# Optimization experiments

Measured on AMD Instinct MI355X. Metric: run time of the kernel, lower is better.

Reference implementation:

```python
import jax, jax.numpy as jnp
import numpy as np

NUM_HEADS = 16


def setup_inputs() -> dict:
    key = jax.random.key(0)
    ks = jax.random.split(key, 5)
    B, S, D = 2, 2048, 1024
    x = jax.random.normal(ks[0], (B, S, D), dtype=jnp.float32)
    # torch Linear weights are [out_features, in_features]; y = x @ W.T + b
    Wq = jax.random.normal(ks[1], (D, D), dtype=jnp.float32) * (D ** -0.5)
    Wk = jax.random.normal(ks[2], (D, D), dtype=jnp.float32) * (D ** -0.5)
    Wv = jax.random.normal(ks[3], (D, D), dtype=jnp.float32) * (D ** -0.5)
    Wo = jax.random.normal(ks[4], (D, D), dtype=jnp.float32) * (D ** -0.5)
    bo = jnp.zeros((D,), dtype=jnp.float32)
    return {"x": x, "Wq": Wq, "Wk": Wk, "Wv": Wv, "Wo": Wo, "bo": bo}


def reference(x, Wq, Wk, Wv, Wo, bo):
    B, S, D = x.shape
    H = NUM_HEADS
    dh = D // H
    # projections (torch Linear: x @ W.T)
    q = (x @ Wq.T).reshape(B, S, H, dh).transpose(0, 2, 1, 3)  # [B,H,S,dh]
    k = (x @ Wk.T).reshape(B, S, H, dh).transpose(0, 2, 1, 3)
    v = (x @ Wv.T).reshape(B, S, H, dh).transpose(0, 2, 1, 3)
    # NOTE: original code takes shape[-1] of the TRANSPOSED key (n,H,dh,S),
    # so the softmax scale is seq_length**-0.5 (a bug we reproduce faithfully).
    scale = jnp.asarray(S, x.dtype) ** -0.5
    scores = jnp.einsum("bhqd,bhkd->bhqk", q, k)  # [B,H,S,S]
    causal = jnp.triu(jnp.ones((S, S), dtype=bool), k=1)
    scores = jnp.where(causal, -jnp.inf, scores * scale)
    weights = jax.nn.softmax(scores, axis=-1)
    # dropout p=0.0 -> identity
    ctx = jnp.einsum("bhqk,bhkd->bhqd", weights, v)  # [B,H,S,dh]
    ctx = ctx.transpose(0, 2, 1, 3).reshape(B, S, D)
    return ctx @ Wo.T + bo
```

## Files before the change

kernel.cpp:

```cpp
#include <hip/hip_runtime.h>
#include <hip/hip_bf16.h>

#define B_SZ    2
#define S_LEN   2048
#define D_MODEL 1024
#define H_NUM   16
#define DH      64
#define M_TOT   (B_SZ * S_LEN)

#define QSCALE (0.022097086912079608f * 1.4426950408889634f)

typedef __attribute__((ext_vector_type(8)))  short          bf16x8;
typedef __attribute__((ext_vector_type(4)))  float          f32x4;
typedef __attribute__((ext_vector_type(16))) float          f32x16;
typedef __attribute__((ext_vector_type(8)))  unsigned short u16x8;
typedef __attribute__((ext_vector_type(4)))  unsigned short u16x4;

__device__ inline unsigned short f2bf(float f) {
  unsigned int u = __float_as_uint(f);
  u += 0x7fffu + ((u >> 16) & 1u);
  return (unsigned short)(u >> 16);
}

__device__ inline float fexp2(float x) {
#if __has_builtin(__builtin_amdgcn_exp2f)
  return __builtin_amdgcn_exp2f(x);
#else
  return exp2f(x);
#endif
}

__device__ inline unsigned cvt_pk_bf16(float lo, float hi) {
  unsigned r;
  asm("v_cvt_pk_bf16_f32 %0, %1, %2" : "=v"(r) : "v"(lo), "v"(hi));
  return r;
}

__device__ inline void gload16(const void* g, void* l) {
  __builtin_amdgcn_global_load_lds(
      (const __attribute__((address_space(1))) void*)g,
      (__attribute__((address_space(3))) void*)l, 16, 0, 0);
}

__global__ __launch_bounds__(256) void to_bf16_all(
    const float* __restrict__ x, const float* __restrict__ wq,
    const float* __restrict__ wk, const float* __restrict__ wv,
    const float* __restrict__ wo, unsigned short* __restrict__ xb,
    unsigned short* __restrict__ wqb, unsigned short* __restrict__ wkb,
    unsigned short* __restrict__ wvb, unsigned short* __restrict__ wob) {
  const size_t i = ((size_t)blockIdx.x * 256 + threadIdx.x) * 8;
  const float* src;
  unsigned short* dst;
  size_t off;
  if (i < 4194304)      { src = x;  dst = xb;  off = i; }
  else if (i < 5242880) { src = wq; dst = wqb; off = i - 4194304; }
  else if (i < 6291456) { src = wk; dst = wkb; off = i - 5242880; }
  else if (i < 7340032) { src = wv; dst = wvb; off = i - 6291456; }
  else                  { src = wo; dst = wob; off = i - 7340032; }
  f32x4 a = *(const f32x4*)(src + off);
  f32x4 b = *(const f32x4*)(src + off + 4);
  u16x8 o;
#pragma unroll
  for (int j = 0; j < 4; j++) { o[j] = f2bf(a[j]); o[4 + j] = f2bf(b[j]); }
  *(u16x8*)(dst + off) = o;
}

__device__ __forceinline__ void gemm_core(const unsigned short* __restrict__ A,
                                          const unsigned short* __restrict__ W,
                                          unsigned short (*Al)[128][32],
                                          unsigned short (*Bl)[128][32],
                                          int mbase, int nbase,
                                          f32x4 acc[4][4]) {
  const int tid  = threadIdx.x;
  const int lane = tid & 63;
  const int wid  = tid >> 6;
  const int wr   = wid >> 1, wc = wid & 1;
  const int g    = lane >> 4, lr = lane & 15;

  const int r0 = tid >> 2;
  const int cg = (tid & 3) ^ ((tid >> 3) & 3);

  const unsigned short* Abase = A + (size_t)(mbase + r0) * D_MODEL + cg * 8;
  const unsigned short* Wbase = W + (size_t)(nbase + r0) * D_MODEL + cg * 8;
  char* ldsA0 = (char*)Al + wid * 1024;
  char* ldsB0 = (char*)Bl + wid * 1024;

  gload16(Abase, ldsA0);
  gload16(Abase + (size_t)64 * D_MODEL, ldsA0 + 4096);
  gload16(Wbase, ldsB0);
  gload16(Wbase + (size_t)64 * D_MODEL, ldsB0 + 4096);

  const int NKT = D_MODEL / 32;
  for (int kt = 0; kt < NKT; ++kt) {
    const int cur = kt & 1;
    if (kt + 1 < NKT) {
      const unsigned short* As = Abase + (kt + 1) * 32;
      const unsigned short* Ws = Wbase + (kt + 1) * 32;
      char* la = ldsA0 + (cur ^ 1) * 8192;
      char* lb = ldsB0 + (cur ^ 1) * 8192;
      gload16(As, la);
      gload16(As + (size_t)64 * D_MODEL, la + 4096);
      gload16(Ws, lb);
      gload16(Ws + (size_t)64 * D_MODEL, lb + 4096);
      asm volatile("s_waitcnt vmcnt(4)" ::: "memory");
    } else {
      asm volatile("s_waitcnt vmcnt(0)" ::: "memory");
    }
    __builtin_amdgcn_s_barrier();

    bf16x8 af[4], bfr[4];
#pragma unroll
    for (int i = 0; i < 4; i++) {
      const int ra = wr * 64 + i * 16 + lr;
      af[i] = *(const bf16x8*)&Al[cur][ra][(g ^ ((ra >> 1) & 3)) * 8];
      const int rb = wc * 64 + i * 16 + lr;
      bfr[i] = *(const bf16x8*)&Bl[cur][rb][(g ^ ((rb >> 1) & 3)) * 8];
    }
    __builtin_amdgcn_s_setprio(1);
#pragma unroll
    for (int i = 0; i < 4; i++)
#pragma unroll
      for (int j = 0; j < 4; j++)
        acc[i][j] = __builtin_amdgcn_mfma_f32_16x16x32_bf16(af[i], bfr[j],
                                                            acc[i][j], 0, 0, 0);
    __builtin_amdgcn_s_setprio(0);
    asm volatile("" ::: "memory");
    __builtin_amdgcn_s_barrier();
  }
}

__global__ __launch_bounds__(256) void gemm_qkv(
    const unsigned short* __restrict__ xb, const unsigned short* __restrict__ wqb,
    const unsigned short* __restrict__ wkb, const unsigned short* __restrict__ wvb,
    unsigned short* __restrict__ qb, unsigned short* __restrict__ kb,
    unsigned short* __restrict__ vt) {
  __shared__ unsigned short Al[2][128][32];
  __shared__ unsigned short Bl[2][128][32];
  const int z = blockIdx.z;
  const unsigned short* W = (z == 0) ? wqb : (z == 1) ? wkb : wvb;
  unsigned short* dst = (z == 0) ? qb : (z == 1) ? kb : vt;
  const float sc = (z == 0) ? QSCALE : 1.0f;

  f32x4 acc[4][4];
#pragma unroll
  for (int i = 0; i < 4; i++)
#pragma unroll
    for (int j = 0; j < 4; j++) acc[i][j] = (f32x4){0.f, 0.f, 0.f, 0.f};

  const int mbase = blockIdx.y * 128, nbase = blockIdx.x * 128;
  gemm_core(xb, W, Al, Bl, mbase, nbase, acc);

  const int lane = threadIdx.x & 63, wid = threadIdx.x >> 6;
  const int wr = wid >> 1, wc = wid & 1, g = lane >> 4, lr = lane & 15;
#pragma unroll
  for (int i = 0; i < 4; i++) {
#pragma unroll
    for (int j = 0; j < 4; j++) {
      const int mg0 = mbase + wr * 64 + i * 16 + g * 4;
      const int ng  = nbase + wc * 64 + j * 16 + lr;
      if (z < 2) {
#pragma unroll
        for (int r = 0; r < 4; r++)
          dst[(size_t)(mg0 + r) * D_MODEL + ng] = f2bf(acc[i][j][r] * sc);
      } else {
        const int hh = ng >> 6, dd = ng & 63;
        const int bb = mg0 >> 11, ss = mg0 & 2047;
        u16x4 pk;
#pragma unroll
        for (int r = 0; r < 4; r++) pk[r] = f2bf(acc[i][j][r]);
        *(u16x4*)&dst[((size_t)((bb * H_NUM + hh) * DH + dd)) * S_LEN + ss] = pk;
      }
    }
  }
}

__global__ __launch_bounds__(256) void gemm_out(
    const unsigned short* __restrict__ cx, const unsigned short* __restrict__ wob,
    float* __restrict__ out, const float* __restrict__ bo) {
  __shared__ unsigned short Al[2][128][32];
  __shared__ unsigned short Bl[2][128][32];
  f32x4 acc[4][4];
#pragma unroll
  for (int i = 0; i < 4; i++)
#pragma unroll
    for (int j = 0; j < 4; j++) acc[i][j] = (f32x4){0.f, 0.f, 0.f, 0.f};

  const int mbase = blockIdx.y * 128, nbase = blockIdx.x * 128;
  gemm_core(cx, wob, Al, Bl, mbase, nbase, acc);

  const int lane = threadIdx.x & 63, wid = threadIdx.x >> 6;
  const int wr = wid >> 1, wc = wid & 1, g = lane >> 4, lr = lane & 15;
#pragma unroll
  for (int i = 0; i < 4; i++) {
#pragma unroll
    for (int j = 0; j < 4; j++) {
      const int mg0 = mbase + wr * 64 + i * 16 + g * 4;
      const int ng  = nbase + wc * 64 + j * 16 + lr;
      const float bv = bo[ng];
#pragma unroll
      for (int r = 0; r < 4; r++)
        out[(size_t)(mg0 + r) * D_MODEL + ng] = acc[i][j][r] + bv;
    }
  }
}

__global__ __launch_bounds__(256) void attn_v3(
    const unsigned short* __restrict__ qb, const unsigned short* __restrict__ kb,
    const unsigned short* __restrict__ vt, unsigned short* __restrict__ cx) {
  __shared__ alignas(16) char smem[32768];

  const int tid  = threadIdx.x;
  const int lane = tid & 63;
  const int w    = tid >> 6;
  const int hi   = lane >> 5;
  const int lq   = lane & 31;
  const int bid  = blockIdx.x;
  const int qi   = (bid < 256) ? (8 + (bid >> 5)) : (7 - ((bid - 256) >> 5));
  const int bh   = bid & 31;
  const int b    = bh >> 4, h = bh & 15;

  const int qg0  = qi * 128 + w * 32;
  const int tok0 = b * S_LEN + qg0;

  const int sr  = tid >> 3;
  const int scg = (tid & 7) ^ (sr & 7);
  const unsigned short* kbase =
      kb + (size_t)(b * S_LEN) * D_MODEL + h * DH + scg * 8;
  const unsigned short* vrow =
      vt + ((size_t)((b * H_NUM + h) * DH + sr)) * S_LEN + scg * 8;
  char* ldsK0 = smem + w * 1024;
  char* ldsV0 = smem + 16384 + w * 1024;

  bf16x8 qf[4];
  {
    const unsigned short* qrow =
        qb + (size_t)(tok0 + lq) * D_MODEL + h * DH + hi * 8;
#pragma unroll
    for (int ks = 0; ks < 4; ks++) qf[ks] = *(const bf16x8*)(qrow + ks * 16);
  }

  f32x16 ctx0, ctx1;
#pragma unroll
  for (int r = 0; r < 16; r++) { ctx0[r] = 0.f; ctx1[r] = 0.f; }
  float m_run = -1e30f, l_run = 0.f;

  const int nkt   = 2 * qi + 2;
  const int ndiag = 2 * qi;

  {
    const unsigned short* sK = kbase + (size_t)sr * D_MODEL;
    gload16(sK, ldsK0);
    gload16(sK + (size_t)32 * D_MODEL, ldsK0 + 4096);
    gload16(vrow, ldsV0);
    gload16(vrow + (size_t)32 * S_LEN, ldsV0 + 4096);
  }

  for (int kt = 0; kt < nkt; ++kt) {
    const int cur = kt & 1;
    if (kt + 1 < nkt) {
      const int nb = cur ^ 1;
      const unsigned short* sK = kbase + (size_t)((kt + 1) * 64 + sr) * D_MODEL;
      gload16(sK, ldsK0 + nb * 8192);
      gload16(sK + (size_t)32 * D_MODEL, ldsK0 + nb * 8192 + 4096);
      const unsigned short* sV = vrow + (kt + 1) * 64;
      gload16(sV, ldsV0 + nb * 8192);
      gload16(sV + (size_t)32 * S_LEN, ldsV0 + nb * 8192 + 4096);
      asm volatile("s_waitcnt vmcnt(4)" ::: "memory");
    } else {
      asm volatile("s_waitcnt vmcnt(0)" ::: "memory");
    }
    __builtin_amdgcn_s_barrier();

    const char* Kc = smem + cur * 8192;
    const char* Vc = smem + 16384 + cur * 8192;

    f32x16 s0, s1;
#pragma unroll
    for (int r = 0; r < 16; r++) { s0[r] = 0.f; s1[r] = 0.f; }
    __builtin_amdgcn_s_setprio(1);
#pragma unroll
    for (int ks = 0; ks < 4; ks++) {
      const int c = ((ks * 2 + hi) ^ (lq & 7)) * 16;
      bf16x8 k0 = *(const bf16x8*)(Kc + lq * 128 + c);
      bf16x8 k1 = *(const bf16x8*)(Kc + (32 + lq) * 128 + c);
      s0 = __builtin_amdgcn_mfma_f32_32x32x16_bf16(k0, qf[ks], s0, 0, 0, 0);
      s1 = __builtin_amdgcn_mfma_f32_32x32x16_bf16(k1, qf[ks], s1, 0, 0, 0);
    }
    __builtin_amdgcn_s_setprio(0);

    if (kt >= ndiag) {
      const int relq = qg0 + lq - kt * 64 - 4 * hi;
#pragma unroll
      for (int r = 0; r < 16; r++) {
        const int ko = (r & 3) + 8 * (r >> 2);
        s0[r] = (ko > relq) ? -1e30f : s0[r];
        s1[r] = (ko + 32 > relq) ? -1e30f : s1[r];
      }
    }

    float pmax = s0[0];
#pragma unroll
    for (int r = 1; r < 16; r++) pmax = fmaxf(pmax, s0[r]);
#pragma unroll
    for (int r = 0; r < 16; r++) pmax = fmaxf(pmax, s1[r]);
    pmax = fmaxf(pmax, __shfl_xor(pmax, 32));

    if (__any(pmax > m_run + 8.0f)) {
      const float mnew = fmaxf(m_run, pmax);
      const float al   = fexp2(m_run - mnew);
      m_run = mnew;
      l_run *= al;
#pragma unroll
      for (int r = 0; r < 16; r++) { ctx0[r] *= al; ctx1[r] *= al; }
    }

    float lsum = 0.f;
#pragma unroll
    for (int ks = 0; ks < 4; ks++) {
      float p[8];
#pragma unroll
      for (int j = 0; j < 8; j++) {
        const int r = (ks & 1) * 8 + j;
        const float sv = (ks < 2) ? s0[r] : s1[r];
        p[j] = fexp2(sv - m_run);
        lsum += p[j];
      }
      const unsigned w01 = cvt_pk_bf16(p[0], p[1]);
      const unsigned w23 = cvt_pk_bf16(p[2], p[3]);
      const unsigned w45 = cvt_pk_bf16(p[4], p[5]);
      const unsigned w67 = cvt_pk_bf16(p[6], p[7]);
      const unsigned x01 = __shfl_xor(w01, 32);
      const unsigned x23 = __shfl_xor(w23, 32);
      const unsigned x45 = __shfl_xor(w45, 32);
      const unsigned x67 = __shfl_xor(w67, 32);
      union { unsigned u[4]; bf16x8 v; } pw;
      pw.u[0] = hi ? x45 : w01;
      pw.u[1] = hi ? x67 : w23;
      pw.u[2] = hi ? w45 : x01;
      pw.u[3] = hi ? w67 : x23;
      const int c = ((ks * 2 + hi) ^ (lq & 7)) * 16;
      bf16x8 v0 = *(const bf16x8*)(Vc + lq * 128 + c);
      bf16x8 v1 = *(const bf16x8*)(Vc + (32 + lq) * 128 + c);
      __builtin_amdgcn_s_setprio(1);
      ctx0 = __builtin_amdgcn_mfma_f32_32x32x16_bf16(v0, pw.v, ctx0, 0, 0, 0);
      ctx1 = __builtin_amdgcn_mfma_f32_32x32x16_bf16(v1, pw.v, ctx1, 0, 0, 0);
      __builtin_amdgcn_s_setprio(0);
    }
    l_run += lsum;
    asm volatile("" ::: "memory");
    __builtin_amdgcn_s_barrier();
  }

  unsigned short (*Tl)[32][72] = (unsigned short (*)[32][72])smem;
  const float lfull = l_run + __shfl_xor(l_run, 32);
  const float inv   = 1.0f / lfull;
#pragma unroll
  for (int rp = 0; rp < 8; rp++) {
    const int r  = rp * 2;
    const int d0 = (r & 3) + 8 * (r >> 2) + 4 * hi;
    *(unsigned*)&Tl[w][lq][d0] = cvt_pk_bf16(ctx0[r] * inv, ctx0[r + 1] * inv);
    *(unsigned*)&Tl[w][lq][32 + d0] =
        cvt_pk_bf16(ctx1[r] * inv, ctx1[r + 1] * inv);
  }
  __builtin_amdgcn_s_waitcnt(0);
  const int q2 = lane >> 1;
#pragma unroll
  for (int i = 0; i < 4; i++) {
    const int ch = (lane & 1) * 4 + i;
    u16x8 vv = *(const u16x8*)&Tl[w][q2][ch * 8];
    *(u16x8*)&cx[(size_t)(tok0 + q2) * D_MODEL + h * DH + ch * 8] = vv;
  }
}

extern "C" void kernel_launch(void* const* d_in, const int* in_sizes, int n_in,
                              void* d_out, int out_size, void* d_ws,
                              size_t ws_size, hipStream_t stream) {
  const float* x  = (const float*)d_in[0];
  const float* Wq = (const float*)d_in[1];
  const float* Wk = (const float*)d_in[2];
  const float* Wv = (const float*)d_in[3];
  const float* Wo = (const float*)d_in[4];
  const float* bo = (const float*)d_in[5];
  float* out = (float*)d_out;

  unsigned short* xb  = (unsigned short*)d_ws;
  unsigned short* wqb = xb  + (size_t)M_TOT * D_MODEL;
  unsigned short* wkb = wqb + (size_t)D_MODEL * D_MODEL;
  unsigned short* wvb = wkb + (size_t)D_MODEL * D_MODEL;
  unsigned short* wob = wvb + (size_t)D_MODEL * D_MODEL;
  unsigned short* qb  = wob + (size_t)D_MODEL * D_MODEL;
  unsigned short* kb  = qb  + (size_t)M_TOT * D_MODEL;
  unsigned short* vt  = kb  + (size_t)M_TOT * D_MODEL;
  unsigned short* cx  = vt  + (size_t)M_TOT * D_MODEL;

  to_bf16_all<<<4096, 256, 0, stream>>>(x, Wq, Wk, Wv, Wo, xb, wqb, wkb, wvb,
                                        wob);
  gemm_qkv<<<dim3(D_MODEL / 128, M_TOT / 128, 3), 256, 0, stream>>>(
      xb, wqb, wkb, wvb, qb, kb, vt);
  attn_v3<<<dim3(512), 256, 0, stream>>>(qb, kb, vt, cx);
  gemm_out<<<dim3(D_MODEL / 128, M_TOT / 128), 256, 0, stream>>>(cx, wob, out,
                                                                 bo);
}
```

Measured before the change: 122.1 us.

## Replace LDS-staged 4-wave attention blocks with single-wave blocks loading K/V into registers

The attention kernel changes from 256-thread blocks that cooperatively stage 64-key K/V tiles in shared memory with barriers to 64-thread single-wave blocks. Each block handles 32 queries and loads 32-key K/V tiles directly from global memory into registers, double-buffered across two register sets. Causal masking only applies on the final diagonal tile. This removes LDS staging and block barriers and gives finer-grained scheduling, longest-first. In exchange, K/V reuse across waves in a block is lost, so global/L2 traffic rises and each wave relies on register prefetch for latency hiding.

```diff
diff --git a/kernel.cpp b/kernel.cpp
--- a/kernel.cpp
+++ b/kernel.cpp
@@ -204,32 +204,26 @@
   }
 }
 
-__global__ __launch_bounds__(256) void attn_v3(
+__global__ __launch_bounds__(64, 3) void attn_v4(
     const unsigned short* __restrict__ qb, const unsigned short* __restrict__ kb,
     const unsigned short* __restrict__ vt, unsigned short* __restrict__ cx) {
-  __shared__ alignas(16) char smem[32768];
-
-  const int tid  = threadIdx.x;
-  const int lane = tid & 63;
-  const int w    = tid >> 6;
+  __shared__ unsigned short Tl[32][72];
+
+  const int lane = threadIdx.x;
   const int hi   = lane >> 5;
   const int lq   = lane & 31;
   const int bid  = blockIdx.x;
-  const int qi   = (bid < 256) ? (8 + (bid >> 5)) : (7 - ((bid - 256) >> 5));
+  const int t    = 63 - (bid >> 5);
   const int bh   = bid & 31;
   const int b    = bh >> 4, h = bh & 15;
 
-  const int qg0  = qi * 128 + w * 32;
+  const int qg0  = t * 32;
   const int tok0 = b * S_LEN + qg0;
 
-  const int sr  = tid >> 3;
-  const int scg = (tid & 7) ^ (sr & 7);
-  const unsigned short* kbase =
-      kb + (size_t)(b * S_LEN) * D_MODEL + h * DH + scg * 8;
-  const unsigned short* vrow =
-      vt + ((size_t)((b * H_NUM + h) * DH + sr)) * S_LEN + scg * 8;
-  char* ldsK0 = smem + w * 1024;
-  char* ldsV0 = smem + 16384 + w * 1024;
+  const unsigned short* kptr =
+      kb + (size_t)(b * S_LEN + lq) * D_MODEL + h * DH + hi * 8;
+  const unsigned short* vptr =
+      vt + ((size_t)((b * H_NUM + h) * DH + lq)) * S_LEN + hi * 8;
 
   bf16x8 qf[4];
   {
@@ -244,65 +238,42 @@
   for (int r = 0; r < 16; r++) { ctx0[r] = 0.f; ctx1[r] = 0.f; }
   float m_run = -1e30f, l_run = 0.f;
 
-  const int nkt   = 2 * qi + 2;
-  const int ndiag = 2 * qi;
-
-  {
-    const unsigned short* sK = kbase + (size_t)sr * D_MODEL;
-    gload16(sK, ldsK0);
-    gload16(sK + (size_t)32 * D_MODEL, ldsK0 + 4096);
-    gload16(vrow, ldsV0);
-    gload16(vrow + (size_t)32 * S_LEN, ldsV0 + 4096);
-  }
-
-  for (int kt = 0; kt < nkt; ++kt) {
-    const int cur = kt & 1;
-    if (kt + 1 < nkt) {
-      const int nb = cur ^ 1;
-      const unsigned short* sK = kbase + (size_t)((kt + 1) * 64 + sr) * D_MODEL;
-      gload16(sK, ldsK0 + nb * 8192);
-      gload16(sK + (size_t)32 * D_MODEL, ldsK0 + nb * 8192 + 4096);
-      const unsigned short* sV = vrow + (kt + 1) * 64;
-      gload16(sV, ldsV0 + nb * 8192);
-      gload16(sV + (size_t)32 * S_LEN, ldsV0 + nb * 8192 + 4096);
-      asm volatile("s_waitcnt vmcnt(4)" ::: "memory");
-    } else {
-      asm volatile("s_waitcnt vmcnt(0)" ::: "memory");
-    }
-    __builtin_amdgcn_s_barrier();
-
-    const char* Kc = smem + cur * 8192;
-    const char* Vc = smem + 16384 + cur * 8192;
-
-    f32x16 s0, s1;
-#pragma unroll
-    for (int r = 0; r < 16; r++) { s0[r] = 0.f; s1[r] = 0.f; }
+  const int nkt = t + 1;
+
+  auto LOADT = [&](bf16x8* kf, bf16x8* vf, int tile) {
+    const unsigned short* ks_ = kptr + (size_t)(tile * 32) * D_MODEL;
+#pragma unroll
+    for (int ks = 0; ks < 4; ks++) kf[ks] = *(const bf16x8*)(ks_ + ks * 16);
+#pragma unroll
+    for (int s2 = 0; s2 < 2; s2++)
+#pragma unroll
+      for (int dh2 = 0; dh2 < 2; dh2++)
+        vf[s2 * 2 + dh2] = *(const bf16x8*)(vptr + (size_t)(dh2 * 32) * S_LEN +
+                                            tile * 32 + s2 * 16);
+  };
+
+  auto COMPUTE = [&](const bf16x8* kf, const bf16x8* vf, int tile) {
+    f32x16 s;
+#pragma unroll
+    for (int r = 0; r < 16; r++) s[r] = 0.f;
     __builtin_amdgcn_s_setprio(1);
 #pragma unroll
-    for (int ks = 0; ks < 4; ks++) {
-      const int c = ((ks * 2 + hi) ^ (lq & 7)) * 16;
-      bf16x8 k0 = *(const bf16x8*)(Kc + lq * 128 + c);
-      bf16x8 k1 = *(const bf16x8*)(Kc + (32 + lq) * 128 + c);
-      s0 = __builtin_amdgcn_mfma_f32_32x32x16_bf16(k0, qf[ks], s0, 0, 0, 0);
-      s1 = __builtin_amdgcn_mfma_f32_32x32x16_bf16(k1, qf[ks], s1, 0, 0, 0);
-    }
+    for (int ks = 0; ks < 4; ks++)
+      s = __builtin_amdgcn_mfma_f32_32x32x16_bf16(kf[ks], qf[ks], s, 0, 0, 0);
     __builtin_amdgcn_s_setprio(0);
 
-    if (kt >= ndiag) {
-      const int relq = qg0 + lq - kt * 64 - 4 * hi;
+    if (tile == t) {
+      const int relq = lq - 4 * hi;
 #pragma unroll
       for (int r = 0; r < 16; r++) {
         const int ko = (r & 3) + 8 * (r >> 2);
-        s0[r] = (ko > relq) ? -1e30f : s0[r];
-        s1[r] = (ko + 32 > relq) ? -1e30f : s1[r];
+        s[r] = (ko > relq) ? -1e30f : s[r];
       }
     }
 
-    float pmax = s0[0];
-#pragma unroll
-    for (int r = 1; r < 16; r++) pmax = fmaxf(pmax, s0[r]);
-#pragma unroll
-    for (int r = 0; r < 16; r++) pmax = fmaxf(pmax, s1[r]);
+    float pmax = s[0];
+#pragma unroll
+    for (int r = 1; r < 16; r++) pmax = fmaxf(pmax, s[r]);
     pmax = fmaxf(pmax, __shfl_xor(pmax, 32));
 
     if (__any(pmax > m_run + 8.0f)) {
@@ -316,13 +287,11 @@
 
     float lsum = 0.f;
 #pragma unroll
-    for (int ks = 0; ks < 4; ks++) {
+    for (int s2 = 0; s2 < 2; s2++) {
       float p[8];
 #pragma unroll
       for (int j = 0; j < 8; j++) {
-        const int r = (ks & 1) * 8 + j;
-        const float sv = (ks < 2) ? s0[r] : s1[r];
-        p[j] = fexp2(sv - m_run);
+        p[j] = fexp2(s[s2 * 8 + j] - m_run);
         lsum += p[j];
       }
       const unsigned w01 = cvt_pk_bf16(p[0], p[1]);
@@ -338,36 +307,44 @@
       pw.u[1] = hi ? x67 : w23;
       pw.u[2] = hi ? w45 : x01;
       pw.u[3] = hi ? w67 : x23;
-      const int c = ((ks * 2 + hi) ^ (lq & 7)) * 16;
-      bf16x8 v0 = *(const bf16x8*)(Vc + lq * 128 + c);
-      bf16x8 v1 = *(const bf16x8*)(Vc + (32 + lq) * 128 + c);
       __builtin_amdgcn_s_setprio(1);
-      ctx0 = __builtin_amdgcn_mfma_f32_32x32x16_bf16(v0, pw.v, ctx0, 0, 0, 0);
-      ctx1 = __builtin_amdgcn_mfma_f32_32x32x16_bf16(v1, pw.v, ctx1, 0, 0, 0);
+      ctx0 = __builtin_amdgcn_mfma_f32_32x32x16_bf16(vf[s2 * 2 + 0], pw.v,
+                                                     ctx0, 0, 0, 0);
+      ctx1 = __builtin_amdgcn_mfma_f32_32x32x16_bf16(vf[s2 * 2 + 1], pw.v,
+                                                     ctx1, 0, 0, 0);
       __builtin_amdgcn_s_setprio(0);
     }
     l_run += lsum;
-    asm volatile("" ::: "memory");
-    __builtin_amdgcn_s_barrier();
-  }
-
-  unsigned short (*Tl)[32][72] = (unsigned short (*)[32][72])smem;
+  };
+
+  bf16x8 kA[4], vA[4], kB[4], vB[4];
+  LOADT(kA, vA, 0);
+  int kt = 0;
+  while (true) {
+    if (kt + 1 < nkt) LOADT(kB, vB, kt + 1);
+    COMPUTE(kA, vA, kt);
+    if (++kt >= nkt) break;
+    if (kt + 1 < nkt) LOADT(kA, vA, kt + 1);
+    COMPUTE(kB, vB, kt);
+    if (++kt >= nkt) break;
+  }
+
   const float lfull = l_run + __shfl_xor(l_run, 32);
   const float inv   = 1.0f / lfull;
 #pragma unroll
   for (int rp = 0; rp < 8; rp++) {
     const int r  = rp * 2;
     const int d0 = (r & 3) + 8 * (r >> 2) + 4 * hi;
-    *(unsigned*)&Tl[w][lq][d0] = cvt_pk_bf16(ctx0[r] * inv, ctx0[r + 1] * inv);
-    *(unsigned*)&Tl[w][lq][32 + d0] =
+    *(unsigned*)&Tl[lq][d0] = cvt_pk_bf16(ctx0[r] * inv, ctx0[r + 1] * inv);
+    *(unsigned*)&Tl[lq][32 + d0] =
         cvt_pk_bf16(ctx1[r] * inv, ctx1[r + 1] * inv);
   }
-  __builtin_amdgcn_s_waitcnt(0);
+  asm volatile("s_waitcnt lgkmcnt(0)" ::: "memory");
   const int q2 = lane >> 1;
 #pragma unroll
   for (int i = 0; i < 4; i++) {
     const int ch = (lane & 1) * 4 + i;
-    u16x8 vv = *(const u16x8*)&Tl[w][q2][ch * 8];
+    u16x8 vv = *(const u16x8*)&Tl[q2][ch * 8];
     *(u16x8*)&cx[(size_t)(tok0 + q2) * D_MODEL + h * DH + ch * 8] = vv;
   }
 }
@@ -397,7 +374,7 @@
                                         wob);
   gemm_qkv<<<dim3(D_MODEL / 128, M_TOT / 128, 3), 256, 0, stream>>>(
       xb, wqb, wkb, wvb, qb, kb, vt);
-  attn_v3<<<dim3(512), 256, 0, stream>>>(qb, kb, vt, cx);
+  attn_v4<<<dim3(2048), 64, 0, stream>>>(qb, kb, vt, cx);
   gemm_out<<<dim3(D_MODEL / 128, M_TOT / 128), 256, 0, stream>>>(cx, wob, out,
                                                                  bo);
 }
```

Result: slower. 146.4 us (+19.8%).

## Split long causal attention rows into two KV partitions with a combine kernel

Applied to the files above, without the earlier changes.

Query tiles 8-15 now have their KV range split into two halves, each run by its own block, so the grid grows from 512 to 768 blocks following a longest-first schedule table. The partial blocks write unnormalized bf16 outputs plus running max and sum into workspace reused from the x/Wq bf16 buffers. A new combine kernel merges the pairs with log-sum-exp weights. The goal is to cut the causal load-imbalance tail, at the cost of an extra launch, partial-output traffic and an extra bf16 rounding. The row max and row sum reductions are also rewritten as trees to shorten dependency chains.

```diff
diff --git a/kernel.cpp b/kernel.cpp
--- a/kernel.cpp
+++ b/kernel.cpp
@@ -20,6 +20,10 @@
   unsigned int u = __float_as_uint(f);
   u += 0x7fffu + ((u >> 16) & 1u);
   return (unsigned short)(u >> 16);
+}
+
+__device__ inline float bf2f(unsigned short u) {
+  return __uint_as_float(((unsigned)u) << 16);
 }
 
 __device__ inline float fexp2(float x) {
@@ -204,9 +208,37 @@
   }
 }
 
-__global__ __launch_bounds__(256) void attn_v3(
+__device__ const unsigned att_sched[24] = {
+    15u | (0u << 8)  | (16u << 16) | (0u << 24),
+    15u | (16u << 8) | (32u << 16) | (1u << 24),
+    7u  | (0u << 8)  | (16u << 16) | (2u << 24),
+    14u | (0u << 8)  | (15u << 16) | (0u << 24),
+    14u | (15u << 8) | (30u << 16) | (1u << 24),
+    13u | (0u << 8)  | (14u << 16) | (0u << 24),
+    13u | (14u << 8) | (28u << 16) | (1u << 24),
+    6u  | (0u << 8)  | (14u << 16) | (2u << 24),
+    12u | (0u << 8)  | (13u << 16) | (0u << 24),
+    12u | (13u << 8) | (26u << 16) | (1u << 24),
+    11u | (0u << 8)  | (12u << 16) | (0u << 24),
+    11u | (12u << 8) | (24u << 16) | (1u << 24),
+    5u  | (0u << 8)  | (12u << 16) | (2u << 24),
+    10u | (0u << 8)  | (11u << 16) | (0u << 24),
+    10u | (11u << 8) | (22u << 16) | (1u << 24),
+    9u  | (0u << 8)  | (10u << 16) | (0u << 24),
+    9u  | (10u << 8) | (20u << 16) | (1u << 24),
+    4u  | (0u << 8)  | (10u << 16) | (2u << 24),
+    8u  | (0u << 8)  | (9u << 16)  | (0u << 24),
+    8u  | (9u << 8)  | (18u << 16) | (1u << 24),
+    3u  | (0u << 8)  | (8u << 16)  | (2u << 24),
+    2u  | (0u << 8)  | (6u << 16)  | (2u << 24),
+    1u  | (0u << 8)  | (4u << 16)  | (2u << 24),
+    0u  | (0u << 8)  | (2u << 16)  | (2u << 24),
+};
+
+__global__ __launch_bounds__(256) void attn_v5(
     const unsigned short* __restrict__ qb, const unsigned short* __restrict__ kb,
-    const unsigned short* __restrict__ vt, unsigned short* __restrict__ cx) {
+    const unsigned short* __restrict__ vt, unsigned short* __restrict__ cx,
+    unsigned short* __restrict__ Opart, float* __restrict__ ml) {
   __shared__ alignas(16) char smem[32768];
 
   const int tid  = threadIdx.x;
@@ -215,7 +247,12 @@
   const int hi   = lane >> 5;
   const int lq   = lane & 31;
   const int bid  = blockIdx.x;
-  const int qi   = (bid < 256) ? (8 + (bid >> 5)) : (7 - ((bid - 256) >> 5));
+
+  const unsigned ent = att_sched[bid >> 5];
+  const int qi   = ent & 255;
+  const int kt0  = (ent >> 8) & 255;
+  const int kt1  = (ent >> 16) & 255;
+  const int part = (ent >> 24) & 255;
   const int bh   = bid & 31;
   const int b    = bh >> 4, h = bh & 15;
 
@@ -244,20 +281,21 @@
   for (int r = 0; r < 16; r++) { ctx0[r] = 0.f; ctx1[r] = 0.f; }
   float m_run = -1e30f, l_run = 0.f;
 
-  const int nkt   = 2 * qi + 2;
   const int ndiag = 2 * qi;
 
   {
-    const unsigned short* sK = kbase + (size_t)sr * D_MODEL;
+    const unsigned short* sK = kbase + (size_t)(kt0 * 64 + sr) * D_MODEL;
     gload16(sK, ldsK0);
     gload16(sK + (size_t)32 * D_MODEL, ldsK0 + 4096);
-    gload16(vrow, ldsV0);
-    gload16(vrow + (size_t)32 * S_LEN, ldsV0 + 4096);
-  }
-
-  for (int kt = 0; kt < nkt; ++kt) {
-    const int cur = kt & 1;
-    if (kt + 1 < nkt) {
+    const unsigned short* sV = vrow + kt0 * 64;
+    gload16(sV, ldsV0);
+    gload16(sV + (size_t)32 * S_LEN, ldsV0 + 4096);
+  }
+
+  int ti = 0;
+  for (int kt = kt0; kt < kt1; ++kt, ++ti) {
+    const int cur = ti & 1;
+    if (kt + 1 < kt1) {
       const int nb = cur ^ 1;
       const unsigned short* sK = kbase + (size_t)((kt + 1) * 64 + sr) * D_MODEL;
       gload16(sK, ldsK0 + nb * 8192);
@@ -298,11 +336,13 @@
       }
     }
 
-    float pmax = s0[0];
-#pragma unroll
-    for (int r = 1; r < 16; r++) pmax = fmaxf(pmax, s0[r]);
-#pragma unroll
-    for (int r = 0; r < 16; r++) pmax = fmaxf(pmax, s1[r]);
+    float tm[8];
+#pragma unroll
+    for (int j = 0; j < 8; j++)
+      tm[j] = fmaxf(fmaxf(s0[j], s0[j + 8]), fmaxf(s1[j], s1[j + 8]));
+#pragma unroll
+    for (int j = 0; j < 4; j++) tm[j] = fmaxf(tm[j], tm[j + 4]);
+    float pmax = fmaxf(fmaxf(tm[0], tm[2]), fmaxf(tm[1], tm[3]));
     pmax = fmaxf(pmax, __shfl_xor(pmax, 32));
 
     if (__any(pmax > m_run + 8.0f)) {
@@ -314,7 +354,7 @@
       for (int r = 0; r < 16; r++) { ctx0[r] *= al; ctx1[r] *= al; }
     }
 
-    float lsum = 0.f;
+    float lsAcc[4];
 #pragma unroll
     for (int ks = 0; ks < 4; ks++) {
       float p[8];
@@ -323,8 +363,9 @@
         const int r = (ks & 1) * 8 + j;
         const float sv = (ks < 2) ? s0[r] : s1[r];
         p[j] = fexp2(sv - m_run);
-        lsum += p[j];
       }
+      lsAcc[ks] = ((p[0] + p[1]) + (p[2] + p[3])) +
+                  ((p[4] + p[5]) + (p[6] + p[7]));
       const unsigned w01 = cvt_pk_bf16(p[0], p[1]);
       const unsigned w23 = cvt_pk_bf16(p[2], p[3]);
       const unsigned w45 = cvt_pk_bf16(p[4], p[5]);
@@ -346,14 +387,14 @@
       ctx1 = __builtin_amdgcn_mfma_f32_32x32x16_bf16(v1, pw.v, ctx1, 0, 0, 0);
       __builtin_amdgcn_s_setprio(0);
     }
-    l_run += lsum;
+    l_run += (lsAcc[0] + lsAcc[1]) + (lsAcc[2] + lsAcc[3]);
     asm volatile("" ::: "memory");
     __builtin_amdgcn_s_barrier();
   }
 
   unsigned short (*Tl)[32][72] = (unsigned short (*)[32][72])smem;
   const float lfull = l_run + __shfl_xor(l_run, 32);
-  const float inv   = 1.0f / lfull;
+  const float inv   = (part == 2) ? (1.0f / lfull) : 1.0f;
 #pragma unroll
   for (int rp = 0; rp < 8; rp++) {
     const int r  = rp * 2;
@@ -362,14 +403,61 @@
     *(unsigned*)&Tl[w][lq][32 + d0] =
         cvt_pk_bf16(ctx1[r] * inv, ctx1[r + 1] * inv);
   }
-  __builtin_amdgcn_s_waitcnt(0);
+  asm volatile("s_waitcnt lgkmcnt(0)" ::: "memory");
   const int q2 = lane >> 1;
-#pragma unroll
-  for (int i = 0; i < 4; i++) {
-    const int ch = (lane & 1) * 4 + i;
-    u16x8 vv = *(const u16x8*)&Tl[w][q2][ch * 8];
-    *(u16x8*)&cx[(size_t)(tok0 + q2) * D_MODEL + h * DH + ch * 8] = vv;
-  }
+  if (part == 2) {
+#pragma unroll
+    for (int i = 0; i < 4; i++) {
+      const int ch = (lane & 1) * 4 + i;
+      u16x8 vv = *(const u16x8*)&Tl[w][q2][ch * 8];
+      *(u16x8*)&cx[(size_t)(tok0 + q2) * D_MODEL + h * DH + ch * 8] = vv;
+    }
+  } else {
+    const int pidx = (qi - 8) * 2 + part;
+    unsigned short* od =
+        Opart + ((size_t)(pidx * 32 + bh) * 128 + w * 32 + q2) * 64;
+#pragma unroll
+    for (int i = 0; i < 4; i++) {
+      const int ch = (lane & 1) * 4 + i;
+      u16x8 vv = *(const u16x8*)&Tl[w][q2][ch * 8];
+      *(u16x8*)&od[ch * 8] = vv;
+    }
+    if (hi == 0) {
+      float2 v2 = make_float2(m_run, lfull);
+      *(float2*)&ml[((size_t)(pidx * 32 + bh) * 128 + w * 32 + lq) * 2] = v2;
+    }
+  }
+}
+
+__global__ __launch_bounds__(256) void attn_combine(
+    const unsigned short* __restrict__ Opart, const float* __restrict__ ml,
+    unsigned short* __restrict__ cx) {
+  const int gid    = blockIdx.x * 256 + threadIdx.x;
+  const int sub    = gid & 7;
+  const int row_id = gid >> 3;
+  const int row    = row_id & 127;
+  const int bh     = (row_id >> 7) & 31;
+  const int qi8    = row_id >> 12;
+  const int pA = qi8 * 2, pB = qi8 * 2 + 1;
+
+  const size_t ra = (size_t)(pA * 32 + bh) * 128 + row;
+  const size_t rb = (size_t)(pB * 32 + bh) * 128 + row;
+  const float mA = ml[ra * 2], lA = ml[ra * 2 + 1];
+  const float mB = ml[rb * 2], lB = ml[rb * 2 + 1];
+  const float m  = fmaxf(mA, mB);
+  const float wA = fexp2(mA - m), wB = fexp2(mB - m);
+  const float inv = 1.0f / (lA * wA + lB * wB);
+
+  u16x8 a = *(const u16x8*)&Opart[ra * 64 + sub * 8];
+  u16x8 c = *(const u16x8*)&Opart[rb * 64 + sub * 8];
+  u16x8 o;
+#pragma unroll
+  for (int j = 0; j < 8; j++)
+    o[j] = f2bf((bf2f(a[j]) * wA + bf2f(c[j]) * wB) * inv);
+
+  const int b = bh >> 4, h = bh & 15;
+  const int tok = b * S_LEN + (qi8 + 8) * 128 + row;
+  *(u16x8*)&cx[(size_t)tok * D_MODEL + h * DH + sub * 8] = o;
 }
 
 extern "C" void kernel_launch(void* const* d_in, const int* in_sizes, int n_in,
@@ -392,12 +480,15 @@
   unsigned short* kb  = qb  + (size_t)M_TOT * D_MODEL;
   unsigned short* vt  = kb  + (size_t)M_TOT * D_MODEL;
   unsigned short* cx  = vt  + (size_t)M_TOT * D_MODEL;
+  unsigned short* Opart = xb;
+  float*          ml    = (float*)wqb;
 
   to_bf16_all<<<4096, 256, 0, stream>>>(x, Wq, Wk, Wv, Wo, xb, wqb, wkb, wvb,
                                         wob);
   gemm_qkv<<<dim3(D_MODEL / 128, M_TOT / 128, 3), 256, 0, stream>>>(
       xb, wqb, wkb, wvb, qb, kb, vt);
-  attn_v3<<<dim3(512), 256, 0, stream>>>(qb, kb, vt, cx);
+  attn_v5<<<dim3(768), 256, 0, stream>>>(qb, kb, vt, cx, Opart, ml);
+  attn_combine<<<dim3(1024), 256, 0, stream>>>(Opart, ml, cx);
   gemm_out<<<dim3(D_MODEL / 128, M_TOT / 128), 256, 0, stream>>>(cx, wob, out,
                                                                  bo);
 }
```

Result: no change. 123.2 us (+0.9%).
